# Kernel tuning notes

Hardware: AMD Instinct MI355X
Metric: run time of the kernel (lower is better)

The kernel has to match this reference:

```python
import jax, jax.numpy as jnp
import numpy as np

BN_EPS = 1e-5
N_IN, N_OUT = 200000, 400000
K, M, C_IN, C_OUT = 27, 100000, 64, 64


def setup_inputs() -> dict:
    key = jax.random.key(0)
    ks = jax.random.split(key, 4)
    x = jax.random.normal(ks[0], (N_IN, C_IN), dtype=jnp.float32)
    W = jax.random.normal(ks[1], (K, C_IN, C_OUT), dtype=jnp.float32) * 0.05
    gamma = jnp.ones((C_OUT,), dtype=jnp.float32)
    beta = jnp.zeros((C_OUT,), dtype=jnp.float32)
    in_idx = jax.random.randint(ks[2], (K, M), 0, N_IN, dtype=jnp.int32)
    out_idx = jax.random.randint(ks[3], (K, M), 0, N_OUT, dtype=jnp.int32)
    return {"x": x, "W": W, "gamma": gamma, "beta": beta,
            "in_idx": in_idx, "out_idx": out_idx, "n_out": N_OUT}


def reference(x, W, gamma, beta, in_idx, out_idx, n_out):
    # Sparse transposed conv via gather-GEMM-scatter over K kernel offsets.
    feats = x[in_idx]                               # [K, M, C_in] gather
    contrib = jnp.einsum('kmi,kio->kmo', feats, W)  # per-offset GEMM
    out = jnp.zeros((n_out, contrib.shape[-1]), dtype=x.dtype)
    out = out.at[out_idx.reshape(-1)].add(contrib.reshape(-1, contrib.shape[-1]))
    # BatchNorm (training-mode batch stats over all output points), gamma=1, beta=0 at init.
    mean = jnp.mean(out, axis=0)
    var = jnp.var(out, axis=0)
    y = (out - mean) * jax.lax.rsqrt(var + BN_EPS) * gamma + beta
    return jax.nn.relu(y)
```

## Files before the change

kernel.cpp:

```cpp
#include <hip/hip_runtime.h>
#include <hip/hip_bf16.h>

#define K_OFF 27
#define M_PTS 100000
#define KM (K_OFF * M_PTS)
#define C_CH 64
#define N_OUT_PTS 400000
#define BN_EPS 1e-5f

#define TILE_PTS 16
#define NT (M_PTS / TILE_PTS)
#define BLKX 64
#define WSTRIDE (BLKX * 4)
#define CAP 40

typedef __attribute__((ext_vector_type(8))) short short8;
typedef __attribute__((ext_vector_type(4))) float f32x4;

__device__ inline short bf16c(float f) {
    return __builtin_bit_cast(short, __float2bfloat16(f));
}
__device__ inline float b2f(unsigned short u) {
    return __builtin_bit_cast(float, (unsigned)u << 16);
}

__device__ inline void pk_atomic_add_bf16(__hip_bfloat16* p, int bits) {
#if __has_builtin(__builtin_amdgcn_global_atomic_fadd_v2bf16)
    typedef short s2v __attribute__((ext_vector_type(2)));
    typedef __attribute__((address_space(1))) s2v* gp;
    s2v v;
    __builtin_memcpy(&v, &bits, 4);
    __builtin_amdgcn_global_atomic_fadd_v2bf16((gp)(unsigned long long)p, v);
#else
    asm volatile("global_atomic_pk_add_bf16 %0, %1, off"
                 :: "v"((unsigned long long)p), "v"(bits) : "memory");
#endif
}

__device__ __attribute__((always_inline)) inline void tile_mfma(
    const float4* cur, const short8 bfrag[2][4], f32x4 acc[4])
{
    short8 af0, af1;
    #pragma unroll
    for (int j = 0; j < 4; ++j) {
        af0[j]     = bf16c(cur[0][j]);
        af0[j + 4] = bf16c(cur[1][j]);
        af1[j]     = bf16c(cur[2][j]);
        af1[j + 4] = bf16c(cur[3][j]);
    }
    #pragma unroll
    for (int tt = 0; tt < 4; ++tt) {
        f32x4 z = {0.f, 0.f, 0.f, 0.f};
        z       = __builtin_amdgcn_mfma_f32_16x16x32_bf16(af0, bfrag[0][tt], z, 0, 0, 0);
        acc[tt] = __builtin_amdgcn_mfma_f32_16x16x32_bf16(af1, bfrag[1][tt], z, 0, 0, 0);
    }
}

__device__ __attribute__((always_inline)) inline void load_bfrag(
    const float* __restrict__ Wk, int g, int c, short8 bfrag[2][4])
{
    #pragma unroll
    for (int s = 0; s < 2; ++s) {
        #pragma unroll
        for (int tt = 0; tt < 4; ++tt) {
            short8 v;
            #pragma unroll
            for (int j = 0; j < 8; ++j)
                v[j] = bf16c(Wk[(size_t)(32 * s + 8 * g + j) * C_CH + 4 * c + tt]);
            bfrag[s][tt] = v;
        }
    }
}


__global__ __launch_bounds__(256) void bin_fill(
    const int* __restrict__ out_idx, int* __restrict__ counts,
    int* __restrict__ entries)
{
    int i = blockIdx.x * 256 + threadIdx.x;
    if (i >= KM) return;
    int o = out_idx[i];
    int pos = atomicAdd(&counts[o], 1);
    if (pos < CAP) entries[(size_t)o * CAP + pos] = i;
}

__global__ __launch_bounds__(256, 4) void contrib_gemm(
    const float* __restrict__ x, const float* __restrict__ W,
    const int* __restrict__ in_idx, unsigned short* __restrict__ contrib)
{
    const int k = blockIdx.y;
    const int lane = threadIdx.x & 63;
    const int wave = threadIdx.x >> 6;
    const int g = lane >> 4;
    const int c = lane & 15;

    short8 bfrag[2][4];
    load_bfrag(W + (size_t)k * C_CH * C_CH, g, c, bfrag);

    const int kbase = k * M_PTS;
    const int t0 = blockIdx.x * 4 + wave;

    int src_c = in_idx[kbase + t0 * TILE_PTS + c];
    float4 cur[4];
    {
        const float4* xr = (const float4*)x + (size_t)src_c * 16;
        cur[0] = xr[2 * g];     cur[1] = xr[2 * g + 1];
        cur[2] = xr[8 + 2 * g]; cur[3] = xr[8 + 2 * g + 1];
    }
    int src_n = (t0 + WSTRIDE < NT) ? in_idx[kbase + (t0 + WSTRIDE) * TILE_PTS + c] : 0;

    int t = t0;
    for (; t + WSTRIDE < NT; t += WSTRIDE) {
        const int tn = t + WSTRIDE;
        float4 nxt[4];
        {
            const float4* xr = (const float4*)x + (size_t)src_n * 16;
            nxt[0] = xr[2 * g];     nxt[1] = xr[2 * g + 1];
            nxt[2] = xr[8 + 2 * g]; nxt[3] = xr[8 + 2 * g + 1];
        }
        const int t2 = tn + WSTRIDE;
        const int src_2 = (t2 < NT) ? in_idx[kbase + t2 * TILE_PTS + c] : 0;

        f32x4 acc[4];
        tile_mfma(cur, bfrag, acc);
        const size_t ebase = (size_t)(kbase + t * TILE_PTS);
        #pragma unroll
        for (int e = 0; e < 4; ++e) {
            union { __hip_bfloat162 h; unsigned u; } p0, p1;
            p0.h = __hip_bfloat162(__float2bfloat16(acc[0][e]), __float2bfloat16(acc[1][e]));
            p1.h = __hip_bfloat162(__float2bfloat16(acc[2][e]), __float2bfloat16(acc[3][e]));
            uint2 wv; wv.x = p0.u; wv.y = p1.u;
            *(uint2*)(contrib + (ebase + 4 * g + e) * C_CH + 4 * c) = wv;
        }

        #pragma unroll
        for (int j = 0; j < 4; ++j) cur[j] = nxt[j];
        src_n = src_2;
    }
    {
        f32x4 acc[4];
        tile_mfma(cur, bfrag, acc);
        const size_t ebase = (size_t)(kbase + t * TILE_PTS);
        #pragma unroll
        for (int e = 0; e < 4; ++e) {
            union { __hip_bfloat162 h; unsigned u; } p0, p1;
            p0.h = __hip_bfloat162(__float2bfloat16(acc[0][e]), __float2bfloat16(acc[1][e]));
            p1.h = __hip_bfloat162(__float2bfloat16(acc[2][e]), __float2bfloat16(acc[3][e]));
            uint2 wv; wv.x = p0.u; wv.y = p1.u;
            *(uint2*)(contrib + (ebase + 4 * g + e) * C_CH + 4 * c) = wv;
        }
    }
}

__global__ __launch_bounds__(256) void gather_bn(
    const unsigned short* __restrict__ contrib, const int* __restrict__ counts,
    const int* __restrict__ entries, float* __restrict__ preact,
    float* __restrict__ stats)
{
    const int lane = threadIdx.x & 63;
    const int wave = threadIdx.x >> 6;
    const int g = lane >> 4;
    const int c4 = lane & 15;

    float s0 = 0.f, s1 = 0.f, s2 = 0.f, s3 = 0.f;
    float q0 = 0.f, q1 = 0.f, q2 = 0.f, q3 = 0.f;

    for (int r = blockIdx.x * 16 + wave * 4 + g; r < N_OUT_PTS; r += gridDim.x * 16) {
        int cnt = counts[r];
        cnt = cnt > CAP ? CAP : cnt;
        const int* ep = entries + (size_t)r * CAP;
        float a0 = 0.f, a1 = 0.f, a2 = 0.f, a3 = 0.f;
        for (int j = 0; j < cnt; ++j) {
            int e = ep[j];
            ushort4 v = *(const ushort4*)(contrib + (size_t)e * C_CH + 4 * c4);
            a0 += b2f(v.x); a1 += b2f(v.y); a2 += b2f(v.z); a3 += b2f(v.w);
        }
        float4 w; w.x = a0; w.y = a1; w.z = a2; w.w = a3;
        *(float4*)(preact + (size_t)r * C_CH + 4 * c4) = w;
        s0 += a0; s1 += a1; s2 += a2; s3 += a3;
        q0 += a0 * a0; q1 += a1 * a1; q2 += a2 * a2; q3 += a3 * a3;
    }

    __shared__ float sh[2][256][4];
    sh[0][threadIdx.x][0] = s0; sh[0][threadIdx.x][1] = s1;
    sh[0][threadIdx.x][2] = s2; sh[0][threadIdx.x][3] = s3;
    sh[1][threadIdx.x][0] = q0; sh[1][threadIdx.x][1] = q1;
    sh[1][threadIdx.x][2] = q2; sh[1][threadIdx.x][3] = q3;
    __syncthreads();
    if (threadIdx.x < C_CH) {
        const int ch = threadIdx.x;
        const int cc = ch >> 2, jj = ch & 3;
        float ts = 0.f, tq = 0.f;
        #pragma unroll
        for (int u = 0; u < 16; ++u) {
            ts += sh[0][16 * u + cc][jj];
            tq += sh[1][16 * u + cc][jj];
        }
        unsafeAtomicAdd(&stats[ch], ts);
        unsafeAtomicAdd(&stats[C_CH + ch], tq);
    }
}

__global__ __launch_bounds__(256) void bn_apply_f32(
    float* __restrict__ out, const float* __restrict__ stats,
    const float* __restrict__ gamma, const float* __restrict__ beta)
{
    const float inv_n = 1.0f / (float)N_OUT_PTS;
    const int c0 = 8 * (threadIdx.x & 7);
    float sc[8], bs[8];
    #pragma unroll
    for (int j = 0; j < 8; ++j) {
        int ch = c0 + j;
        float mean = stats[ch] * inv_n;
        float var = stats[C_CH + ch] * inv_n - mean * mean;
        float s = gamma[ch] * rsqrtf(var + BN_EPS);
        sc[j] = s;
        bs[j] = beta[ch] - mean * s;
    }
    float4* o4 = (float4*)out;
    const size_t n = (size_t)N_OUT_PTS * C_CH / 8;
    const size_t stride = (size_t)gridDim.x * blockDim.x;
    for (size_t i = (size_t)blockIdx.x * blockDim.x + threadIdx.x; i < n; i += stride) {
        float4 r0 = o4[2 * i], r1 = o4[2 * i + 1];
        r0.x = fmaxf(fmaf(r0.x, sc[0], bs[0]), 0.f);
        r0.y = fmaxf(fmaf(r0.y, sc[1], bs[1]), 0.f);
        r0.z = fmaxf(fmaf(r0.z, sc[2], bs[2]), 0.f);
        r0.w = fmaxf(fmaf(r0.w, sc[3], bs[3]), 0.f);
        r1.x = fmaxf(fmaf(r1.x, sc[4], bs[4]), 0.f);
        r1.y = fmaxf(fmaf(r1.y, sc[5], bs[5]), 0.f);
        r1.z = fmaxf(fmaf(r1.z, sc[6], bs[6]), 0.f);
        r1.w = fmaxf(fmaf(r1.w, sc[7], bs[7]), 0.f);
        o4[2 * i] = r0;
        o4[2 * i + 1] = r1;
    }
}

__global__ __launch_bounds__(256, 4) void scatter_gemm_fb(
    const float* __restrict__ x, const float* __restrict__ W,
    const int* __restrict__ in_idx, const int* __restrict__ out_idx,
    __hip_bfloat16* __restrict__ out_ws)
{
    const int k = blockIdx.y;
    const int lane = threadIdx.x & 63;
    const int wave = threadIdx.x >> 6;
    const int g = lane >> 4;
    const int c = lane & 15;

    short8 bfrag[2][4];
    load_bfrag(W + (size_t)k * C_CH * C_CH, g, c, bfrag);

    const int kbase = k * M_PTS;
    for (int t = blockIdx.x * 4 + wave; t < NT; t += WSTRIDE) {
        int src = in_idx[kbase + t * TILE_PTS + c];
        float4 cur[4];
        const float4* xr = (const float4*)x + (size_t)src * 16;
        cur[0] = xr[2 * g];     cur[1] = xr[2 * g + 1];
        cur[2] = xr[8 + 2 * g]; cur[3] = xr[8 + 2 * g + 1];
        int dstv[4];
        #pragma unroll
        for (int e = 0; e < 4; ++e)
            dstv[e] = out_idx[kbase + t * TILE_PTS + 4 * g + e];
        f32x4 acc[4];
        tile_mfma(cur, bfrag, acc);
        #pragma unroll
        for (int e = 0; e < 4; ++e) {
            __hip_bfloat16* rp = out_ws + (size_t)dstv[e] * C_CH + 4 * c;
            union { __hip_bfloat162 h; int i; } p0, p1;
            p0.h = __hip_bfloat162(__float2bfloat16(acc[0][e]), __float2bfloat16(acc[1][e]));
            p1.h = __hip_bfloat162(__float2bfloat16(acc[2][e]), __float2bfloat16(acc[3][e]));
            pk_atomic_add_bf16(rp, p0.i);
            pk_atomic_add_bf16(rp + 2, p1.i);
        }
    }
}

__global__ __launch_bounds__(256) void bn_stats_fb(
    const __hip_bfloat16* __restrict__ ws, float* __restrict__ stats)
{
    const uint4* in = (const uint4*)ws;
    const size_t n = (size_t)N_OUT_PTS * C_CH / 8;
    const size_t stride = (size_t)gridDim.x * blockDim.x;
    float s[8], s2[8];
    #pragma unroll
    for (int j = 0; j < 8; ++j) { s[j] = 0.f; s2[j] = 0.f; }
    for (size_t i = (size_t)blockIdx.x * blockDim.x + threadIdx.x; i < n; i += stride) {
        uint4 q = in[i];
        unsigned wds[4] = {q.x, q.y, q.z, q.w};
        #pragma unroll
        for (int j = 0; j < 4; ++j) {
            __hip_bfloat162 h = *(__hip_bfloat162*)&wds[j];
            float f0 = __low2float(h), f1 = __high2float(h);
            s[2 * j] += f0;  s2[2 * j] += f0 * f0;
            s[2 * j + 1] += f1; s2[2 * j + 1] += f1 * f1;
        }
    }
    __shared__ float sh[2][256][8];
    #pragma unroll
    for (int j = 0; j < 8; ++j) { sh[0][threadIdx.x][j] = s[j]; sh[1][threadIdx.x][j] = s2[j]; }
    __syncthreads();
    if (threadIdx.x < C_CH) {
        const int c = threadIdx.x;
        float ts = 0.f, t2 = 0.f;
        #pragma unroll
        for (int q = 0; q < 32; ++q) {
            ts += sh[0][8 * q + (c >> 3)][c & 7];
            t2 += sh[1][8 * q + (c >> 3)][c & 7];
        }
        unsafeAtomicAdd(&stats[c], ts);
        unsafeAtomicAdd(&stats[C_CH + c], t2);
    }
}

__global__ __launch_bounds__(256) void bn_apply_fb(
    const __hip_bfloat16* __restrict__ ws, const float* __restrict__ stats,
    const float* __restrict__ gamma, const float* __restrict__ beta,
    float* __restrict__ out)
{
    const float inv_n = 1.0f / (float)N_OUT_PTS;
    const int c0 = 8 * (threadIdx.x & 7);
    float sc[8], bs[8];
    #pragma unroll
    for (int j = 0; j < 8; ++j) {
        int c = c0 + j;
        float mean = stats[c] * inv_n;
        float var = stats[C_CH + c] * inv_n - mean * mean;
        float s = gamma[c] * rsqrtf(var + BN_EPS);
        sc[j] = s;
        bs[j] = beta[c] - mean * s;
    }
    const uint4* in = (const uint4*)ws;
    float4* o4 = (float4*)out;
    const size_t n = (size_t)N_OUT_PTS * C_CH / 8;
    const size_t stride = (size_t)gridDim.x * blockDim.x;
    for (size_t i = (size_t)blockIdx.x * blockDim.x + threadIdx.x; i < n; i += stride) {
        uint4 q = in[i];
        unsigned wds[4] = {q.x, q.y, q.z, q.w};
        float f[8];
        #pragma unroll
        for (int j = 0; j < 4; ++j) {
            __hip_bfloat162 h = *(__hip_bfloat162*)&wds[j];
            f[2 * j] = __low2float(h);
            f[2 * j + 1] = __high2float(h);
        }
        float4 r0, r1;
        r0.x = fmaxf(fmaf(f[0], sc[0], bs[0]), 0.f);
        r0.y = fmaxf(fmaf(f[1], sc[1], bs[1]), 0.f);
        r0.z = fmaxf(fmaf(f[2], sc[2], bs[2]), 0.f);
        r0.w = fmaxf(fmaf(f[3], sc[3], bs[3]), 0.f);
        r1.x = fmaxf(fmaf(f[4], sc[4], bs[4]), 0.f);
        r1.y = fmaxf(fmaf(f[5], sc[5], bs[5]), 0.f);
        r1.z = fmaxf(fmaf(f[6], sc[6], bs[6]), 0.f);
        r1.w = fmaxf(fmaf(f[7], sc[7], bs[7]), 0.f);
        o4[2 * i] = r0;
        o4[2 * i + 1] = r1;
    }
}

extern "C" void kernel_launch(void* const* d_in, const int* in_sizes, int n_in,
                              void* d_out, int out_size, void* d_ws, size_t ws_size,
                              hipStream_t stream) {
    const float* x      = (const float*)d_in[0];
    const float* W      = (const float*)d_in[1];
    const float* gamma  = (const float*)d_in[2];
    const float* beta   = (const float*)d_in[3];
    const int*   in_idx = (const int*)d_in[4];
    const int*   out_idx= (const int*)d_in[5];
    float* out = (float*)d_out;

    const size_t CONTRIB_B = (size_t)KM * C_CH * 2;
    const size_t COUNTS_B  = (size_t)N_OUT_PTS * 4;
    const size_t ENTRIES_B = (size_t)N_OUT_PTS * CAP * 4;
    const size_t STATS_B   = 2 * C_CH * sizeof(float);
    const size_t NEEDED = CONTRIB_B + COUNTS_B + ENTRIES_B + STATS_B;

    if (ws_size >= NEEDED) {
        unsigned short* contrib = (unsigned short*)d_ws;
        int* counts = (int*)((char*)d_ws + CONTRIB_B);
        int* entries = (int*)((char*)d_ws + CONTRIB_B + COUNTS_B);
        float* stats = (float*)((char*)d_ws + CONTRIB_B + COUNTS_B + ENTRIES_B);

        (void)hipMemsetAsync(counts, 0, COUNTS_B, stream);
        (void)hipMemsetAsync(stats, 0, STATS_B, stream);

        bin_fill<<<(KM + 255) / 256, 256, 0, stream>>>(out_idx, counts, entries);
        contrib_gemm<<<dim3(BLKX, K_OFF), 256, 0, stream>>>(x, W, in_idx, contrib);
        gather_bn<<<12800, 256, 0, stream>>>(contrib, counts, entries, out, stats);
        bn_apply_f32<<<2048, 256, 0, stream>>>(out, stats, gamma, beta);
    } else {
        __hip_bfloat16* out_ws = (__hip_bfloat16*)d_ws;
        const size_t acc_elems = (size_t)N_OUT_PTS * C_CH;
        float* stats = (float*)((char*)d_ws + acc_elems * sizeof(__hip_bfloat16));
        const size_t clear_bytes = acc_elems * sizeof(__hip_bfloat16) + STATS_B;
        (void)hipMemsetAsync(d_ws, 0, clear_bytes, stream);

        scatter_gemm_fb<<<dim3(BLKX, K_OFF), 256, 0, stream>>>(x, W, in_idx, out_idx, out_ws);
        bn_stats_fb<<<2048, 256, 0, stream>>>(out_ws, stats);
        bn_apply_fb<<<2048, 256, 0, stream>>>(out_ws, stats, gamma, beta, out);
    }
}
```

Measured before the change: 768.0 us.

## Fuse gather-GEMM into output-stationary accumulation with CSR-sorted input lists

Replaces the materialized bf16 contrib buffer with an output-stationary scheme. A per-row, per-offset byte histogram and a two-level scan build a CSR list of input indices grouped by output row and offset. A fused kernel then gathers x rows for each 16-row output tile and accumulates MFMA products per offset in registers before writing preact and BN stats. This removes the large contrib write and reread and the fixed-capacity bins. In exchange it adds hist, scan and fill passes, and lanes in a tile diverge because rows have different per-offset counts, which wastes MFMA work. A byte counter per offset also assumes no more than 255 hits per row per offset.

```diff
diff --git a/kernel.cpp b/kernel.cpp
--- a/kernel.cpp
+++ b/kernel.cpp
@@ -7,21 +7,13 @@
 #define C_CH 64
 #define N_OUT_PTS 400000
 #define BN_EPS 1e-5f
-
-#define TILE_PTS 16
-#define NT (M_PTS / TILE_PTS)
-#define BLKX 64
-#define WSTRIDE (BLKX * 4)
-#define CAP 40
+#define N_TILES (N_OUT_PTS / 16)
 
 typedef __attribute__((ext_vector_type(8))) short short8;
 typedef __attribute__((ext_vector_type(4))) float f32x4;
 
 __device__ inline short bf16c(float f) {
     return __builtin_bit_cast(short, __float2bfloat16(f));
-}
-__device__ inline float b2f(unsigned short u) {
-    return __builtin_bit_cast(float, (unsigned)u << 16);
 }
 
 __device__ inline void pk_atomic_add_bf16(__hip_bfloat16* p, int bits) {
@@ -37,28 +29,105 @@
 #endif
 }
 
-__device__ __attribute__((always_inline)) inline void tile_mfma(
-    const float4* cur, const short8 bfrag[2][4], f32x4 acc[4])
-{
-    short8 af0, af1;
-    #pragma unroll
-    for (int j = 0; j < 4; ++j) {
-        af0[j]     = bf16c(cur[0][j]);
-        af0[j + 4] = bf16c(cur[1][j]);
-        af1[j]     = bf16c(cur[2][j]);
-        af1[j + 4] = bf16c(cur[3][j]);
-    }
-    #pragma unroll
-    for (int tt = 0; tt < 4; ++tt) {
-        f32x4 z = {0.f, 0.f, 0.f, 0.f};
-        z       = __builtin_amdgcn_mfma_f32_16x16x32_bf16(af0, bfrag[0][tt], z, 0, 0, 0);
-        acc[tt] = __builtin_amdgcn_mfma_f32_16x16x32_bf16(af1, bfrag[1][tt], z, 0, 0, 0);
-    }
-}
-
-__device__ __attribute__((always_inline)) inline void load_bfrag(
-    const float* __restrict__ Wk, int g, int c, short8 bfrag[2][4])
-{
+__device__ inline unsigned bytesum(unsigned v) {
+    return (v & 255u) + ((v >> 8) & 255u) + ((v >> 16) & 255u) + (v >> 24);
+}
+
+
+__global__ __launch_bounds__(256) void hist_kernel(
+    const int* __restrict__ out_idx, unsigned* __restrict__ hist)
+{
+    int i = blockIdx.x * 256 + threadIdx.x;
+    if (i >= KM) return;
+    int row = out_idx[i];
+    int k = i / M_PTS;
+    atomicAdd(&hist[(size_t)row * 8 + (k >> 2)], 1u << (8 * (k & 3)));
+}
+
+__global__ __launch_bounds__(256) void scan_a(
+    const unsigned* __restrict__ hist, int* __restrict__ partial,
+    int* __restrict__ blockSums)
+{
+    __shared__ int sh[256];
+    const int t = threadIdx.x, b = blockIdx.x;
+    const int r0 = b * 1024 + t * 4;
+    int cnt[4] = {0, 0, 0, 0};
+    if (r0 < N_OUT_PTS) {
+        #pragma unroll
+        for (int u = 0; u < 4; ++u) {
+            const uint4* hp = (const uint4*)(hist + (size_t)(r0 + u) * 8);
+            uint4 a = hp[0], bq = hp[1];
+            cnt[u] = (int)(bytesum(a.x) + bytesum(a.y) + bytesum(a.z) + bytesum(a.w) +
+                           bytesum(bq.x) + bytesum(bq.y) + bytesum(bq.z) + bytesum(bq.w));
+        }
+    }
+    int tsum = cnt[0] + cnt[1] + cnt[2] + cnt[3];
+    sh[t] = tsum;
+    __syncthreads();
+    for (int o = 1; o < 256; o <<= 1) {
+        int u = (t >= o) ? sh[t - o] : 0;
+        __syncthreads();
+        sh[t] += u;
+        __syncthreads();
+    }
+    int excl = sh[t] - tsum;
+    if (r0 < N_OUT_PTS) {
+        partial[r0]     = excl;
+        partial[r0 + 1] = excl + cnt[0];
+        partial[r0 + 2] = excl + cnt[0] + cnt[1];
+        partial[r0 + 3] = excl + cnt[0] + cnt[1] + cnt[2];
+    }
+    if (t == 255) blockSums[b] = sh[255];
+}
+
+#define SCAN_BLOCKS ((N_OUT_PTS + 1023) / 1024)
+
+__global__ __launch_bounds__(512) void scan_b(
+    const int* __restrict__ blockSums, int* __restrict__ blockOff)
+{
+    __shared__ int sh[512];
+    const int t = threadIdx.x;
+    int v = (t < SCAN_BLOCKS) ? blockSums[t] : 0;
+    sh[t] = v;
+    __syncthreads();
+    for (int o = 1; o < 512; o <<= 1) {
+        int u = (t >= o) ? sh[t - o] : 0;
+        __syncthreads();
+        sh[t] += u;
+        __syncthreads();
+    }
+    if (t < SCAN_BLOCKS) blockOff[t] = sh[t] - v;
+}
+
+__global__ __launch_bounds__(256) void fill_kernel(
+    const int* __restrict__ out_idx, const int* __restrict__ in_idx,
+    const unsigned* __restrict__ hist, unsigned* __restrict__ cursor,
+    const int* __restrict__ partial, const int* __restrict__ blockOff,
+    int* __restrict__ entries)
+{
+    int i = blockIdx.x * 256 + threadIdx.x;
+    if (i >= KM) return;
+    int row = out_idx[i];
+    int k = i / M_PTS;
+    const unsigned* hw = hist + (size_t)row * 8;
+    int w = k >> 2, r = k & 3;
+    int pre = 0;
+    for (int q = 0; q < w; ++q) pre += (int)bytesum(hw[q]);
+    unsigned v = hw[w];
+    for (int b = 0; b < r; ++b) pre += (int)((v >> (8 * b)) & 255u);
+    unsigned old = atomicAdd(&cursor[(size_t)row * 8 + w], 1u << (8 * r));
+    int inK = (int)((old >> (8 * r)) & 255u);
+    int pos = partial[row] + blockOff[row >> 10] + pre + inK;
+    entries[pos] = in_idx[i];
+}
+
+__global__ __launch_bounds__(64) void prepack_B(
+    const float* __restrict__ W, unsigned short* __restrict__ packedB)
+{
+    const int k = blockIdx.x;
+    const int lane = threadIdx.x;
+    const int g = lane >> 4, c = lane & 15;
+    const float* __restrict__ Wk = W + (size_t)k * C_CH * C_CH;
     #pragma unroll
     for (int s = 0; s < 2; ++s) {
         #pragma unroll
@@ -67,125 +136,135 @@
             #pragma unroll
             for (int j = 0; j < 8; ++j)
                 v[j] = bf16c(Wk[(size_t)(32 * s + 8 * g + j) * C_CH + 4 * c + tt]);
-            bfrag[s][tt] = v;
-        }
-    }
-}
-
-
-__global__ __launch_bounds__(256) void bin_fill(
-    const int* __restrict__ out_idx, int* __restrict__ counts,
-    int* __restrict__ entries)
-{
-    int i = blockIdx.x * 256 + threadIdx.x;
-    if (i >= KM) return;
-    int o = out_idx[i];
-    int pos = atomicAdd(&counts[o], 1);
-    if (pos < CAP) entries[(size_t)o * CAP + pos] = i;
-}
-
-__global__ __launch_bounds__(256, 4) void contrib_gemm(
-    const float* __restrict__ x, const float* __restrict__ W,
-    const int* __restrict__ in_idx, unsigned short* __restrict__ contrib)
-{
-    const int k = blockIdx.y;
+            *(short8*)(packedB + ((size_t)(k * 64 + lane)) * 64 + (s * 4 + tt) * 8) = v;
+        }
+    }
+}
+
+__global__ __launch_bounds__(256) void gather_bn_fused(
+    const float* __restrict__ x, const unsigned short* __restrict__ packedB,
+    const int* __restrict__ entries, const int* __restrict__ partial,
+    const int* __restrict__ blockOff, const unsigned* __restrict__ hist,
+    float* __restrict__ preact, float* __restrict__ stats)
+{
     const int lane = threadIdx.x & 63;
     const int wave = threadIdx.x >> 6;
-    const int g = lane >> 4;
-    const int c = lane & 15;
-
-    short8 bfrag[2][4];
-    load_bfrag(W + (size_t)k * C_CH * C_CH, g, c, bfrag);
-
-    const int kbase = k * M_PTS;
-    const int t0 = blockIdx.x * 4 + wave;
-
-    int src_c = in_idx[kbase + t0 * TILE_PTS + c];
-    float4 cur[4];
+    const int g = lane >> 4, c = lane & 15;
+    const int gw = blockIdx.x * 4 + wave;
+    const int tileA = 2 * gw, tileB = 2 * gw + 1;
+    const int rowA = tileA * 16 + c;
+    const int rowB = tileB * 16 + c;
+
+    int ptrA = partial[rowA] + blockOff[rowA >> 10];
+    int ptrB = partial[rowB] + blockOff[rowB >> 10];
+
+    float4 nxA[4], nxB[4];
     {
-        const float4* xr = (const float4*)x + (size_t)src_c * 16;
-        cur[0] = xr[2 * g];     cur[1] = xr[2 * g + 1];
-        cur[2] = xr[8 + 2 * g]; cur[3] = xr[8 + 2 * g + 1];
-    }
-    int src_n = (t0 + WSTRIDE < NT) ? in_idx[kbase + (t0 + WSTRIDE) * TILE_PTS + c] : 0;
-
-    int t = t0;
-    for (; t + WSTRIDE < NT; t += WSTRIDE) {
-        const int tn = t + WSTRIDE;
-        float4 nxt[4];
+        int iA = ptrA < KM ? ptrA : KM;
+        int iB = ptrB < KM ? ptrB : KM;
+        int sA = entries[iA];
+        const float4* xr = (const float4*)x + (size_t)sA * 16;
+        nxA[0] = xr[2 * g];     nxA[1] = xr[2 * g + 1];
+        nxA[2] = xr[8 + 2 * g]; nxA[3] = xr[8 + 2 * g + 1];
+        int sB = entries[iB];
+        const float4* xs = (const float4*)x + (size_t)sB * 16;
+        nxB[0] = xs[2 * g];     nxB[1] = xs[2 * g + 1];
+        nxB[2] = xs[8 + 2 * g]; nxB[3] = xs[8 + 2 * g + 1];
+    }
+
+    f32x4 accA[4], accB[4];
+    #pragma unroll
+    for (int tt = 0; tt < 4; ++tt) {
+        accA[tt] = (f32x4){0.f, 0.f, 0.f, 0.f};
+        accB[tt] = (f32x4){0.f, 0.f, 0.f, 0.f};
+    }
+
+    for (int k = 0; k < K_OFF; ++k) {
+        short8 bfrag[8];
         {
-            const float4* xr = (const float4*)x + (size_t)src_n * 16;
-            nxt[0] = xr[2 * g];     nxt[1] = xr[2 * g + 1];
-            nxt[2] = xr[8 + 2 * g]; nxt[3] = xr[8 + 2 * g + 1];
-        }
-        const int t2 = tn + WSTRIDE;
-        const int src_2 = (t2 < NT) ? in_idx[kbase + t2 * TILE_PTS + c] : 0;
-
-        f32x4 acc[4];
-        tile_mfma(cur, bfrag, acc);
-        const size_t ebase = (size_t)(kbase + t * TILE_PTS);
-        #pragma unroll
-        for (int e = 0; e < 4; ++e) {
-            union { __hip_bfloat162 h; unsigned u; } p0, p1;
-            p0.h = __hip_bfloat162(__float2bfloat16(acc[0][e]), __float2bfloat16(acc[1][e]));
-            p1.h = __hip_bfloat162(__float2bfloat16(acc[2][e]), __float2bfloat16(acc[3][e]));
-            uint2 wv; wv.x = p0.u; wv.y = p1.u;
-            *(uint2*)(contrib + (ebase + 4 * g + e) * C_CH + 4 * c) = wv;
-        }
-
-        #pragma unroll
-        for (int j = 0; j < 4; ++j) cur[j] = nxt[j];
-        src_n = src_2;
-    }
-    {
-        f32x4 acc[4];
-        tile_mfma(cur, bfrag, acc);
-        const size_t ebase = (size_t)(kbase + t * TILE_PTS);
-        #pragma unroll
-        for (int e = 0; e < 4; ++e) {
-            union { __hip_bfloat162 h; unsigned u; } p0, p1;
-            p0.h = __hip_bfloat162(__float2bfloat16(acc[0][e]), __float2bfloat16(acc[1][e]));
-            p1.h = __hip_bfloat162(__float2bfloat16(acc[2][e]), __float2bfloat16(acc[3][e]));
-            uint2 wv; wv.x = p0.u; wv.y = p1.u;
-            *(uint2*)(contrib + (ebase + 4 * g + e) * C_CH + 4 * c) = wv;
-        }
-    }
-}
-
-__global__ __launch_bounds__(256) void gather_bn(
-    const unsigned short* __restrict__ contrib, const int* __restrict__ counts,
-    const int* __restrict__ entries, float* __restrict__ preact,
-    float* __restrict__ stats)
-{
-    const int lane = threadIdx.x & 63;
-    const int wave = threadIdx.x >> 6;
-    const int g = lane >> 4;
-    const int c4 = lane & 15;
-
-    float s0 = 0.f, s1 = 0.f, s2 = 0.f, s3 = 0.f;
-    float q0 = 0.f, q1 = 0.f, q2 = 0.f, q3 = 0.f;
-
-    for (int r = blockIdx.x * 16 + wave * 4 + g; r < N_OUT_PTS; r += gridDim.x * 16) {
-        int cnt = counts[r];
-        cnt = cnt > CAP ? CAP : cnt;
-        const int* ep = entries + (size_t)r * CAP;
-        float a0 = 0.f, a1 = 0.f, a2 = 0.f, a3 = 0.f;
-        for (int j = 0; j < cnt; ++j) {
-            int e = ep[j];
-            ushort4 v = *(const ushort4*)(contrib + (size_t)e * C_CH + 4 * c4);
-            a0 += b2f(v.x); a1 += b2f(v.y); a2 += b2f(v.z); a3 += b2f(v.w);
-        }
-        float4 w; w.x = a0; w.y = a1; w.z = a2; w.w = a3;
-        *(float4*)(preact + (size_t)r * C_CH + 4 * c4) = w;
-        s0 += a0; s1 += a1; s2 += a2; s3 += a3;
-        q0 += a0 * a0; q1 += a1 * a1; q2 += a2 * a2; q3 += a3 * a3;
+            const short8* bp = (const short8*)packedB + (size_t)(k * 64 + lane) * 8;
+            #pragma unroll
+            for (int f = 0; f < 8; ++f) bfrag[f] = bp[f];
+        }
+        const int sh8 = 8 * (k & 3);
+        int rA = (int)((hist[(size_t)rowA * 8 + (k >> 2)] >> sh8) & 255u);
+        int rB = (int)((hist[(size_t)rowB * 8 + (k >> 2)] >> sh8) & 255u);
+
+        int j = 0;
+        while (__any(j < rA)) {
+            bool act = j < rA;
+            short8 af0 = {0, 0, 0, 0, 0, 0, 0, 0};
+            short8 af1 = {0, 0, 0, 0, 0, 0, 0, 0};
+            if (act) {
+                #pragma unroll
+                for (int q = 0; q < 4; ++q) {
+                    af0[q]     = bf16c(nxA[0][q]);
+                    af0[q + 4] = bf16c(nxA[1][q]);
+                    af1[q]     = bf16c(nxA[2][q]);
+                    af1[q + 4] = bf16c(nxA[3][q]);
+                }
+                ++ptrA;
+                int s_ = entries[ptrA];
+                const float4* xr = (const float4*)x + (size_t)s_ * 16;
+                nxA[0] = xr[2 * g];     nxA[1] = xr[2 * g + 1];
+                nxA[2] = xr[8 + 2 * g]; nxA[3] = xr[8 + 2 * g + 1];
+            }
+            #pragma unroll
+            for (int tt = 0; tt < 4; ++tt) {
+                f32x4 z = __builtin_amdgcn_mfma_f32_16x16x32_bf16(af0, bfrag[tt], accA[tt], 0, 0, 0);
+                accA[tt] = __builtin_amdgcn_mfma_f32_16x16x32_bf16(af1, bfrag[4 + tt], z, 0, 0, 0);
+            }
+            ++j;
+        }
+        j = 0;
+        while (__any(j < rB)) {
+            bool act = j < rB;
+            short8 af0 = {0, 0, 0, 0, 0, 0, 0, 0};
+            short8 af1 = {0, 0, 0, 0, 0, 0, 0, 0};
+            if (act) {
+                #pragma unroll
+                for (int q = 0; q < 4; ++q) {
+                    af0[q]     = bf16c(nxB[0][q]);
+                    af0[q + 4] = bf16c(nxB[1][q]);
+                    af1[q]     = bf16c(nxB[2][q]);
+                    af1[q + 4] = bf16c(nxB[3][q]);
+                }
+                ++ptrB;
+                int s_ = entries[ptrB];
+                const float4* xs = (const float4*)x + (size_t)s_ * 16;
+                nxB[0] = xs[2 * g];     nxB[1] = xs[2 * g + 1];
+                nxB[2] = xs[8 + 2 * g]; nxB[3] = xs[8 + 2 * g + 1];
+            }
+            #pragma unroll
+            for (int tt = 0; tt < 4; ++tt) {
+                f32x4 z = __builtin_amdgcn_mfma_f32_16x16x32_bf16(af0, bfrag[tt], accB[tt], 0, 0, 0);
+                accB[tt] = __builtin_amdgcn_mfma_f32_16x16x32_bf16(af1, bfrag[4 + tt], z, 0, 0, 0);
+            }
+            ++j;
+        }
+    }
+
+    float s[4] = {0.f, 0.f, 0.f, 0.f}, q[4] = {0.f, 0.f, 0.f, 0.f};
+    #pragma unroll
+    for (int e = 0; e < 4; ++e) {
+        float4 w;
+        w.x = accA[0][e]; w.y = accA[1][e]; w.z = accA[2][e]; w.w = accA[3][e];
+        *(float4*)(preact + (size_t)(tileA * 16 + 4 * g + e) * C_CH + 4 * c) = w;
+        s[0] += w.x; s[1] += w.y; s[2] += w.z; s[3] += w.w;
+        q[0] += w.x * w.x; q[1] += w.y * w.y; q[2] += w.z * w.z; q[3] += w.w * w.w;
+        float4 u;
+        u.x = accB[0][e]; u.y = accB[1][e]; u.z = accB[2][e]; u.w = accB[3][e];
+        *(float4*)(preact + (size_t)(tileB * 16 + 4 * g + e) * C_CH + 4 * c) = u;
+        s[0] += u.x; s[1] += u.y; s[2] += u.z; s[3] += u.w;
+        q[0] += u.x * u.x; q[1] += u.y * u.y; q[2] += u.z * u.z; q[3] += u.w * u.w;
     }
 
     __shared__ float sh[2][256][4];
-    sh[0][threadIdx.x][0] = s0; sh[0][threadIdx.x][1] = s1;
-    sh[0][threadIdx.x][2] = s2; sh[0][threadIdx.x][3] = s3;
-    sh[1][threadIdx.x][0] = q0; sh[1][threadIdx.x][1] = q1;
-    sh[1][threadIdx.x][2] = q2; sh[1][threadIdx.x][3] = q3;
+    #pragma unroll
+    for (int tt = 0; tt < 4; ++tt) {
+        sh[0][threadIdx.x][tt] = s[tt];
+        sh[1][threadIdx.x][tt] = q[tt];
+    }
     __syncthreads();
     if (threadIdx.x < C_CH) {
         const int ch = threadIdx.x;
@@ -213,9 +292,9 @@
         int ch = c0 + j;
         float mean = stats[ch] * inv_n;
         float var = stats[C_CH + ch] * inv_n - mean * mean;
-        float s = gamma[ch] * rsqrtf(var + BN_EPS);
-        sc[j] = s;
-        bs[j] = beta[ch] - mean * s;
+        float sfac = gamma[ch] * rsqrtf(var + BN_EPS);
+        sc[j] = sfac;
+        bs[j] = beta[ch] - mean * sfac;
     }
     float4* o4 = (float4*)out;
     const size_t n = (size_t)N_OUT_PTS * C_CH / 8;
@@ -235,6 +314,27 @@
     }
 }
 
+#define TILE_PTS 16
+#define NT (M_PTS / TILE_PTS)
+#define FB_BLKX 64
+#define FB_WSTRIDE (FB_BLKX * 4)
+
+__device__ __attribute__((always_inline)) inline void load_bfrag_fb(
+    const float* __restrict__ Wk, int g, int c, short8 bfrag[2][4])
+{
+    #pragma unroll
+    for (int s = 0; s < 2; ++s) {
+        #pragma unroll
+        for (int tt = 0; tt < 4; ++tt) {
+            short8 v;
+            #pragma unroll
+            for (int j = 0; j < 8; ++j)
+                v[j] = bf16c(Wk[(size_t)(32 * s + 8 * g + j) * C_CH + 4 * c + tt]);
+            bfrag[s][tt] = v;
+        }
+    }
+}
+
 __global__ __launch_bounds__(256, 4) void scatter_gemm_fb(
     const float* __restrict__ x, const float* __restrict__ W,
     const int* __restrict__ in_idx, const int* __restrict__ out_idx,
@@ -243,25 +343,33 @@
     const int k = blockIdx.y;
     const int lane = threadIdx.x & 63;
     const int wave = threadIdx.x >> 6;
-    const int g = lane >> 4;
-    const int c = lane & 15;
-
+    const int g = lane >> 4, c = lane & 15;
     short8 bfrag[2][4];
-    load_bfrag(W + (size_t)k * C_CH * C_CH, g, c, bfrag);
-
+    load_bfrag_fb(W + (size_t)k * C_CH * C_CH, g, c, bfrag);
     const int kbase = k * M_PTS;
-    for (int t = blockIdx.x * 4 + wave; t < NT; t += WSTRIDE) {
+    for (int t = blockIdx.x * 4 + wave; t < NT; t += FB_WSTRIDE) {
         int src = in_idx[kbase + t * TILE_PTS + c];
+        const float4* xr = (const float4*)x + (size_t)src * 16;
         float4 cur[4];
-        const float4* xr = (const float4*)x + (size_t)src * 16;
         cur[0] = xr[2 * g];     cur[1] = xr[2 * g + 1];
         cur[2] = xr[8 + 2 * g]; cur[3] = xr[8 + 2 * g + 1];
         int dstv[4];
         #pragma unroll
         for (int e = 0; e < 4; ++e)
             dstv[e] = out_idx[kbase + t * TILE_PTS + 4 * g + e];
+        short8 af0, af1;
+        #pragma unroll
+        for (int j = 0; j < 4; ++j) {
+            af0[j] = bf16c(cur[0][j]); af0[j + 4] = bf16c(cur[1][j]);
+            af1[j] = bf16c(cur[2][j]); af1[j + 4] = bf16c(cur[3][j]);
+        }
         f32x4 acc[4];
-        tile_mfma(cur, bfrag, acc);
+        #pragma unroll
+        for (int tt = 0; tt < 4; ++tt) {
+            f32x4 z = {0.f, 0.f, 0.f, 0.f};
+            z       = __builtin_amdgcn_mfma_f32_16x16x32_bf16(af0, bfrag[0][tt], z, 0, 0, 0);
+            acc[tt] = __builtin_amdgcn_mfma_f32_16x16x32_bf16(af1, bfrag[1][tt], z, 0, 0, 0);
+        }
         #pragma unroll
         for (int e = 0; e < 4; ++e) {
             __hip_bfloat16* rp = out_ws + (size_t)dstv[e] * C_CH + 4 * c;
@@ -284,8 +392,8 @@
     #pragma unroll
     for (int j = 0; j < 8; ++j) { s[j] = 0.f; s2[j] = 0.f; }
     for (size_t i = (size_t)blockIdx.x * blockDim.x + threadIdx.x; i < n; i += stride) {
-        uint4 q = in[i];
-        unsigned wds[4] = {q.x, q.y, q.z, q.w};
+        uint4 qv = in[i];
+        unsigned wds[4] = {qv.x, qv.y, qv.z, qv.w};
         #pragma unroll
         for (int j = 0; j < 4; ++j) {
             __hip_bfloat162 h = *(__hip_bfloat162*)&wds[j];
@@ -299,15 +407,15 @@
     for (int j = 0; j < 8; ++j) { sh[0][threadIdx.x][j] = s[j]; sh[1][threadIdx.x][j] = s2[j]; }
     __syncthreads();
     if (threadIdx.x < C_CH) {
-        const int c = threadIdx.x;
+        const int cch = threadIdx.x;
         float ts = 0.f, t2 = 0.f;
         #pragma unroll
-        for (int q = 0; q < 32; ++q) {
-            ts += sh[0][8 * q + (c >> 3)][c & 7];
-            t2 += sh[1][8 * q + (c >> 3)][c & 7];
-        }
-        unsafeAtomicAdd(&stats[c], ts);
-        unsafeAtomicAdd(&stats[C_CH + c], t2);
+        for (int u = 0; u < 32; ++u) {
+            ts += sh[0][8 * u + (cch >> 3)][cch & 7];
+            t2 += sh[1][8 * u + (cch >> 3)][cch & 7];
+        }
+        unsafeAtomicAdd(&stats[cch], ts);
+        unsafeAtomicAdd(&stats[C_CH + cch], t2);
     }
 }
 
@@ -321,20 +429,20 @@
     float sc[8], bs[8];
     #pragma unroll
     for (int j = 0; j < 8; ++j) {
-        int c = c0 + j;
-        float mean = stats[c] * inv_n;
-        float var = stats[C_CH + c] * inv_n - mean * mean;
-        float s = gamma[c] * rsqrtf(var + BN_EPS);
-        sc[j] = s;
-        bs[j] = beta[c] - mean * s;
+        int ch = c0 + j;
+        float mean = stats[ch] * inv_n;
+        float var = stats[C_CH + ch] * inv_n - mean * mean;
+        float sfac = gamma[ch] * rsqrtf(var + BN_EPS);
+        sc[j] = sfac;
+        bs[j] = beta[ch] - mean * sfac;
     }
     const uint4* in = (const uint4*)ws;
     float4* o4 = (float4*)out;
     const size_t n = (size_t)N_OUT_PTS * C_CH / 8;
     const size_t stride = (size_t)gridDim.x * blockDim.x;
     for (size_t i = (size_t)blockIdx.x * blockDim.x + threadIdx.x; i < n; i += stride) {
-        uint4 q = in[i];
-        unsigned wds[4] = {q.x, q.y, q.z, q.w};
+        uint4 qv = in[i];
+        unsigned wds[4] = {qv.x, qv.y, qv.z, qv.w};
         float f[8];
         #pragma unroll
         for (int j = 0; j < 4; ++j) {
@@ -367,33 +475,50 @@
     const int*   out_idx= (const int*)d_in[5];
     float* out = (float*)d_out;
 
-    const size_t CONTRIB_B = (size_t)KM * C_CH * 2;
-    const size_t COUNTS_B  = (size_t)N_OUT_PTS * 4;
-    const size_t ENTRIES_B = (size_t)N_OUT_PTS * CAP * 4;
-    const size_t STATS_B   = 2 * C_CH * sizeof(float);
-    const size_t NEEDED = CONTRIB_B + COUNTS_B + ENTRIES_B + STATS_B;
+    auto al = [](size_t v) { return (v + 255) & ~(size_t)255; };
+    size_t off = 0;
+    const size_t entries_off = off; off += al((size_t)(KM + 64) * 4);
+    const size_t partial_off = off; off += al((size_t)N_OUT_PTS * 4);
+    const size_t zero_start  = off;
+    const size_t hist_off    = off; off += al((size_t)N_OUT_PTS * 32);
+    const size_t cursor_off  = off; off += al((size_t)N_OUT_PTS * 32);
+    const size_t bsum_off    = off; off += al(512 * 4);
+    const size_t boff_off    = off; off += al(512 * 4);
+    const size_t stats_off   = off; off += al(2 * C_CH * sizeof(float));
+    const size_t zero_end    = off;
+    const size_t packB_off   = off; off += al((size_t)K_OFF * 64 * 128);
+    const size_t NEEDED = off;
 
     if (ws_size >= NEEDED) {
-        unsigned short* contrib = (unsigned short*)d_ws;
-        int* counts = (int*)((char*)d_ws + CONTRIB_B);
-        int* entries = (int*)((char*)d_ws + CONTRIB_B + COUNTS_B);
-        float* stats = (float*)((char*)d_ws + CONTRIB_B + COUNTS_B + ENTRIES_B);
-
-        (void)hipMemsetAsync(counts, 0, COUNTS_B, stream);
-        (void)hipMemsetAsync(stats, 0, STATS_B, stream);
-
-        bin_fill<<<(KM + 255) / 256, 256, 0, stream>>>(out_idx, counts, entries);
-        contrib_gemm<<<dim3(BLKX, K_OFF), 256, 0, stream>>>(x, W, in_idx, contrib);
-        gather_bn<<<12800, 256, 0, stream>>>(contrib, counts, entries, out, stats);
+        char* wsb = (char*)d_ws;
+        int*      entries = (int*)(wsb + entries_off);
+        int*      partial = (int*)(wsb + partial_off);
+        unsigned* hist    = (unsigned*)(wsb + hist_off);
+        unsigned* cursor  = (unsigned*)(wsb + cursor_off);
+        int*      bsum    = (int*)(wsb + bsum_off);
+        int*      boff    = (int*)(wsb + boff_off);
+        float*    stats   = (float*)(wsb + stats_off);
+        unsigned short* packB = (unsigned short*)(wsb + packB_off);
+
+        (void)hipMemsetAsync(wsb + zero_start, 0, zero_end - zero_start, stream);
+        (void)hipMemsetAsync(entries + KM, 0, 64 * sizeof(int), stream);
+
+        prepack_B<<<K_OFF, 64, 0, stream>>>(W, packB);
+        hist_kernel<<<(KM + 255) / 256, 256, 0, stream>>>(out_idx, hist);
+        scan_a<<<SCAN_BLOCKS, 256, 0, stream>>>(hist, partial, bsum);
+        scan_b<<<1, 512, 0, stream>>>(bsum, boff);
+        fill_kernel<<<(KM + 255) / 256, 256, 0, stream>>>(
+            out_idx, in_idx, hist, cursor, partial, boff, entries);
+        gather_bn_fused<<<N_TILES / 8, 256, 0, stream>>>(
+            x, packB, entries, partial, boff, hist, out, stats);
         bn_apply_f32<<<2048, 256, 0, stream>>>(out, stats, gamma, beta);
     } else {
         __hip_bfloat16* out_ws = (__hip_bfloat16*)d_ws;
         const size_t acc_elems = (size_t)N_OUT_PTS * C_CH;
         float* stats = (float*)((char*)d_ws + acc_elems * sizeof(__hip_bfloat16));
-        const size_t clear_bytes = acc_elems * sizeof(__hip_bfloat16) + STATS_B;
+        const size_t clear_bytes = acc_elems * sizeof(__hip_bfloat16) + 2 * C_CH * sizeof(float);
         (void)hipMemsetAsync(d_ws, 0, clear_bytes, stream);
-
-        scatter_gemm_fb<<<dim3(BLKX, K_OFF), 256, 0, stream>>>(x, W, in_idx, out_idx, out_ws);
+        scatter_gemm_fb<<<dim3(FB_BLKX, K_OFF), 256, 0, stream>>>(x, W, in_idx, out_idx, out_ws);
         bn_stats_fb<<<2048, 256, 0, stream>>>(out_ws, stats);
         bn_apply_fb<<<2048, 256, 0, stream>>>(out_ws, stats, gamma, beta, out);
     }
```

Result: slower. 1.189 ms (+54.8%).
